# Optimization experiments

Hardware: AMD Instinct MI355X
Metric: run time of the kernel (lower is better)

## Reference

```python
import jax, jax.numpy as jnp
import numpy as np

B, L, D, H = 2, 2048, 1024, 16
HD = D // H
SCALE = HD ** (-0.5)


def setup_inputs() -> dict:
    key = jax.random.key(0)
    ks = jax.random.split(key, 12)
    mk = lambda k, shape: (0.02 * jax.random.normal(k, shape, dtype=jnp.float32))
    return {
        "x_real": jax.random.normal(ks[0], (B, L, D), dtype=jnp.float32),
        "x_imag": jax.random.normal(ks[1], (B, L, D), dtype=jnp.float32),
        "wq_r": mk(ks[2], (D, D)),
        "wq_i": mk(ks[3], (D, D)),
        "wk_r": mk(ks[4], (D, D)),
        "wk_i": mk(ks[5], (D, D)),
        "wv_r": mk(ks[6], (D, D)),
        "wv_i": mk(ks[7], (D, D)),
        "wo_r": mk(ks[8], (D, D)),
        "wo_i": mk(ks[9], (D, D)),
        "bo_r": jnp.zeros((D,), dtype=jnp.float32),
        "bo_i": jnp.zeros((D,), dtype=jnp.float32),
    }


def _clinear(xr, xi, wr, wi):
    # (a+bi)(c+di): real = a@Wr^T - b@Wi^T ; imag = a@Wi^T + b@Wr^T
    r = xr @ wr.T - xi @ wi.T
    i = xr @ wi.T + xi @ wr.T
    return r, i


def _heads(t):
    # [B,L,D] -> [B,H,L,hd]
    return t.reshape(B, L, H, HD).transpose(0, 2, 1, 3)


def reference(x_real, x_imag, wq_r, wq_i, wk_r, wk_i, wv_r, wv_i, wo_r, wo_i, bo_r, bo_i):
    Qr, Qi = _clinear(x_real, x_imag, wq_r, wq_i)
    Kr, Ki = _clinear(x_real, x_imag, wk_r, wk_i)
    Vr, Vi = _clinear(x_real, x_imag, wv_r, wv_i)
    Qr, Qi, Kr, Ki, Vr, Vi = map(_heads, (Qr, Qi, Kr, Ki, Vr, Vi))

    # real part of complex dot product: Re(Q)Re(K)^T + Im(Q)Im(K)^T
    scores = (jnp.einsum("bhqd,bhkd->bhqk", Qr, Kr)
              + jnp.einsum("bhqd,bhkd->bhqk", Qi, Ki)) * SCALE
    causal = jnp.tril(jnp.ones((L, L), dtype=bool))
    scores = jnp.where(causal, scores, -jnp.inf)
    w = jax.nn.softmax(scores, axis=-1)

    out_r = jnp.einsum("bhqk,bhkd->bhqd", w, Vr)
    out_i = jnp.einsum("bhqk,bhkd->bhqd", w, Vi)
    merge = lambda t: t.transpose(0, 2, 1, 3).reshape(B, L, D)
    out_r, out_i = merge(out_r), merge(out_i)

    yr, yi = _clinear(out_r, out_i, wo_r, wo_i)
    return yr + bo_r, yi + bo_i
```

## Files before the change

kernel.cpp:

```cpp
#include <hip/hip_runtime.h>
#include <hip/hip_bf16.h>


using f32x4  = __attribute__((ext_vector_type(4))) float;
using short8 = __attribute__((ext_vector_type(8))) short;
using bf16_t = __hip_bfloat16;

#define AS1 __attribute__((address_space(1)))
#define AS3 __attribute__((address_space(3)))

__device__ __forceinline__ void gload_lds16(const bf16_t* g, bf16_t* l) {
  __builtin_amdgcn_global_load_lds((const AS1 unsigned int*)g, (AS3 unsigned int*)l, 16, 0, 0);
}

__device__ __forceinline__ unsigned short bfbits(float f) {
  union { bf16_t h; unsigned short u; } c; c.h = __float2bfloat16(f); return c.u;
}

__global__ void pack_x_k(const float* __restrict__ xr, const float* __restrict__ xi,
                         bf16_t* __restrict__ out) {
  const int total4 = 4096 * 2048 / 4;
  for (int idx = blockIdx.x * blockDim.x + threadIdx.x; idx < total4;
       idx += gridDim.x * blockDim.x) {
    int m = idx >> 9, k = (idx & 511) * 4;
    const float* src = (k < 1024) ? (xr + (size_t)m * 1024 + k)
                                  : (xi + (size_t)m * 1024 + (k - 1024));
    float4 v = *(const float4*)src;
    unsigned int lo = (unsigned)bfbits(v.x) | ((unsigned)bfbits(v.y) << 16);
    unsigned int hi = (unsigned)bfbits(v.z) | ((unsigned)bfbits(v.w) << 16);
    *(uint2*)(out + (size_t)idx * 4) = make_uint2(lo, hi);
  }
}

__global__ void pack_wqkv_k(const float* __restrict__ wqr, const float* __restrict__ wqi,
                            const float* __restrict__ wkr, const float* __restrict__ wki,
                            const float* __restrict__ wvr, const float* __restrict__ wvi,
                            bf16_t* __restrict__ out) {
  const int total4 = 6144 * 2048 / 4;
  for (int idx = blockIdx.x * blockDim.x + threadIdx.x; idx < total4;
       idx += gridDim.x * blockDim.x) {
    int row = idx >> 9, k = (idx & 511) * 4;
    int sec = row >> 10, r1 = row & 1023;
    bool lowk = (k < 1024);
    int kk = lowk ? k : (k - 1024);
    const float* base = wqr; float sg = 1.f;
    switch (sec) {
      case 0: base = lowk ? wqr : wqi; sg = lowk ? 1.f : -1.f; break;
      case 1: base = lowk ? wqi : wqr; break;
      case 2: base = lowk ? wkr : wki; sg = lowk ? 1.f : -1.f; break;
      case 3: base = lowk ? wki : wkr; break;
      case 4: base = lowk ? wvr : wvi; sg = lowk ? 1.f : -1.f; break;
      case 5: base = lowk ? wvi : wvr; break;
    }
    float4 v = *(const float4*)(base + (size_t)r1 * 1024 + kk);
    unsigned int lo = (unsigned)bfbits(v.x * sg) | ((unsigned)bfbits(v.y * sg) << 16);
    unsigned int hi = (unsigned)bfbits(v.z * sg) | ((unsigned)bfbits(v.w * sg) << 16);
    *(uint2*)(out + (size_t)idx * 4) = make_uint2(lo, hi);
  }
}

__global__ void pack_wo_k(const float* __restrict__ wor, const float* __restrict__ woi,
                          bf16_t* __restrict__ out) {
  const int total4 = 2048 * 2048 / 4;
  for (int idx = blockIdx.x * blockDim.x + threadIdx.x; idx < total4;
       idx += gridDim.x * blockDim.x) {
    int row = idx >> 9, k = (idx & 511) * 4;
    int sec = row >> 10, r1 = row & 1023;
    bool lowk = (k < 1024);
    int kk = lowk ? k : (k - 1024);
    const float* base; float sg = 1.f;
    if (sec == 0) { base = lowk ? wor : woi; sg = lowk ? 1.f : -1.f; }
    else          { base = lowk ? woi : wor; }
    float4 v = *(const float4*)(base + (size_t)r1 * 1024 + kk);
    unsigned int lo = (unsigned)bfbits(v.x * sg) | ((unsigned)bfbits(v.y * sg) << 16);
    unsigned int hi = (unsigned)bfbits(v.z * sg) | ((unsigned)bfbits(v.w * sg) << 16);
    *(uint2*)(out + (size_t)idx * 4) = make_uint2(lo, hi);
  }
}

__device__ __forceinline__ void gemm_core(const bf16_t* __restrict__ A,
                                          const bf16_t* __restrict__ W,
                                          int m0, int n0, f32x4 (&acc)[4][4]) {
  __shared__ __align__(16) bf16_t sA[128 * 64];
  __shared__ __align__(16) bf16_t sB[128 * 64];
  const int tid = threadIdx.x;
  const int lane = tid & 63, w = tid >> 6;
  const int wr = w >> 1, wc = w & 1;
  const int quad = lane >> 4, m16 = lane & 15;
  const int srow = w * 32 + (lane >> 3);
  const int gcol = (((lane & 7) ^ (lane >> 3)) * 8);
  const int swz7 = m16 & 7;
  for (int k0 = 0; k0 < 2048; k0 += 64) {
    __syncthreads();
#pragma unroll
    for (int i = 0; i < 4; ++i) {
      gload_lds16(A + (size_t)(m0 + srow + i * 8) * 2048 + k0 + gcol,
                  sA + (size_t)(w * 32 + i * 8) * 64 + lane * 8);
      gload_lds16(W + (size_t)(n0 + srow + i * 8) * 2048 + k0 + gcol,
                  sB + (size_t)(w * 32 + i * 8) * 64 + lane * 8);
    }
    __syncthreads();
#pragma unroll
    for (int kk = 0; kk < 2; ++kk) {
      short8 af[4], bf[4];
#pragma unroll
      for (int i = 0; i < 4; ++i)
        af[i] = *(const short8*)(sA + (wr * 64 + i * 16 + m16) * 64 +
                                 ((kk * 4 + quad) ^ swz7) * 8);
#pragma unroll
      for (int j = 0; j < 4; ++j)
        bf[j] = *(const short8*)(sB + (wc * 64 + j * 16 + m16) * 64 +
                                 ((kk * 4 + quad) ^ swz7) * 8);
#pragma unroll
      for (int i = 0; i < 4; ++i)
#pragma unroll
        for (int j = 0; j < 4; ++j)
          acc[i][j] = __builtin_amdgcn_mfma_f32_16x16x32_bf16(af[i], bf[j], acc[i][j], 0, 0, 0);
    }
  }
}

__global__ __launch_bounds__(256) void gemm_qkv_k(const bf16_t* __restrict__ A,
                                                  const bf16_t* __restrict__ W,
                                                  bf16_t* __restrict__ qk,
                                                  bf16_t* __restrict__ vt) {
  f32x4 acc[4][4] = {};
  const int m0 = blockIdx.x * 128, n0 = blockIdx.y * 128;
  gemm_core(A, W, m0, n0, acc);
  const int lane = threadIdx.x & 63, w = threadIdx.x >> 6;
  const int wr = w >> 1, wc = w & 1, quad = lane >> 4, m16 = lane & 15;
#pragma unroll
  for (int i = 0; i < 4; ++i) {
    const int rowb = m0 + wr * 64 + i * 16 + quad * 4;
#pragma unroll
    for (int j = 0; j < 4; ++j) {
      const int col = n0 + wc * 64 + j * 16 + m16;
      if (col < 4096) {
        const float sc = (col < 2048) ? 0.125f : 1.f;
#pragma unroll
        for (int r = 0; r < 4; ++r)
          qk[(size_t)(rowb + r) * 4096 + col] = __float2bfloat16(acc[i][j][r] * sc);
      } else {
        const int vcol = col - 4096;
        const int ri = vcol >> 10, dfeat = vcol & 1023;
        const int b = rowb >> 11, seq = rowb & 2047;
        const size_t vrow = (size_t)(b * 2048 + (dfeat >> 6) * 128 + ri * 64 + (dfeat & 63));
        unsigned int lo = (unsigned)bfbits(acc[i][j][0]) | ((unsigned)bfbits(acc[i][j][1]) << 16);
        unsigned int hi = (unsigned)bfbits(acc[i][j][2]) | ((unsigned)bfbits(acc[i][j][3]) << 16);
        *(uint2*)(vt + vrow * 2048 + seq) = make_uint2(lo, hi);
      }
    }
  }
}

__global__ __launch_bounds__(256) void gemm_out_k(const bf16_t* __restrict__ A,
                                                  const bf16_t* __restrict__ W,
                                                  const float* __restrict__ bor,
                                                  const float* __restrict__ boi,
                                                  float* __restrict__ out) {
  f32x4 acc[4][4] = {};
  const int m0 = blockIdx.x * 128, n0 = blockIdx.y * 128;
  gemm_core(A, W, m0, n0, acc);
  const int lane = threadIdx.x & 63, w = threadIdx.x >> 6;
  const int wr = w >> 1, wc = w & 1, quad = lane >> 4, m16 = lane & 15;
#pragma unroll
  for (int i = 0; i < 4; ++i) {
    const int rowb = m0 + wr * 64 + i * 16 + quad * 4;
#pragma unroll
    for (int j = 0; j < 4; ++j) {
      const int col = n0 + wc * 64 + j * 16 + m16;
      float bias; float* op;
      if (col < 1024) { bias = bor[col]; op = out + col; }
      else            { bias = boi[col - 1024]; op = out + 4194304 + (col - 1024); }
#pragma unroll
      for (int r = 0; r < 4; ++r)
        op[(size_t)(rowb + r) * 1024] = acc[i][j][r] + bias;
    }
  }
}

__global__ __launch_bounds__(256, 2) void attn_k(const bf16_t* __restrict__ qk,
                                                 const bf16_t* __restrict__ vt,
                                                 bf16_t* __restrict__ acat) {
  __shared__ __align__(16) bf16_t sK[64 * 128];
  __shared__ __align__(16) bf16_t sV[144 * 64];
  __shared__ __align__(16) bf16_t sP[4][2][16 * 72];
  const int tid = threadIdx.x, lane = tid & 63, w = tid >> 6;
  const int quad = lane >> 4, m16 = lane & 15;
  const int x = blockIdx.x, bh = blockIdx.y, b = bh >> 4, h = bh & 15;
  const size_t qkrow0 = (size_t)b * 2048;
  const int qA = x * 64, qB = (31 - x) * 64;
  const int nT = 32 - x;
  const int swz7 = m16 & 7;

  {
    const int rr = tid >> 4, cb = (tid & 15) * 4;
    const bf16_t v = __float2bfloat16(rr == 0 ? 1.f : 0.f);
#pragma unroll
    for (int i = 0; i < 4; ++i) sV[(128 + rr) * 64 + cb + i] = v;
  }

  short8 qfA[4], qfB[4];
  {
    const bf16_t* qa = qk + (qkrow0 + qA + w * 16 + m16) * 4096;
    const bf16_t* qb = qk + (qkrow0 + qB + w * 16 + m16) * 4096;
#pragma unroll
    for (int kk = 0; kk < 4; ++kk) {
      const int col = (kk >> 1) * 1024 + h * 64 + (kk & 1) * 32 + quad * 8;
      qfA[kk] = *(const short8*)(qa + col);
      qfB[kk] = *(const short8*)(qb + col);
    }
  }
  f32x4 oA[9], oB[9];
#pragma unroll
  for (int j = 0; j < 9; ++j) { oA[j] = (f32x4){0.f,0.f,0.f,0.f}; oB[j] = (f32x4){0.f,0.f,0.f,0.f}; }

  const int qrowA = qA + w * 16 + quad * 4;
  const int qrowB = qB + w * 16 + quad * 4;

  const int kl4 = lane >> 4, kl15 = lane & 15;
  const int vl3 = lane >> 3;
  const int vg7 = ((lane & 7) ^ vl3) * 8;

  for (int t = 0; t < nT; ++t) {
    const int k0 = t * 64;
    __syncthreads();
#pragma unroll
    for (int i = 0; i < 4; ++i) {
      const int row = w * 16 + i * 4 + kl4;
      const int g = kl15 ^ (row & 7);
      const int col = 2048 + (g >> 3) * 1024 + h * 64 + (g & 7) * 8;
      gload_lds16(qk + (qkrow0 + k0 + row) * 4096 + col,
                  sK + (size_t)(w * 16 + i * 4) * 128 + lane * 8);
    }
#pragma unroll
    for (int i = 0; i < 4; ++i) {
      const int row = w * 32 + i * 8 + vl3;
      gload_lds16(vt + ((size_t)bh * 128 + row) * 2048 + k0 + vg7,
                  sV + (size_t)(w * 32 + i * 8) * 64 + lane * 8);
    }
    __syncthreads();

    const bool aAct = (t <= x);
    const bool dgA = (t == x), dgB = (t == nT - 1);

    f32x4 sAv[4], sBv[4];
    if (aAct) {
#pragma unroll
      for (int jt = 0; jt < 4; ++jt) {
        f32x4 a1 = (f32x4){0.f,0.f,0.f,0.f}, a2 = (f32x4){0.f,0.f,0.f,0.f};
#pragma unroll
        for (int kk = 0; kk < 4; ++kk) {
          short8 kf = *(const short8*)(sK + (jt * 16 + m16) * 128 +
                                       ((kk * 4 + quad) ^ swz7) * 8);
          a1 = __builtin_amdgcn_mfma_f32_16x16x32_bf16(qfA[kk], kf, a1, 0, 0, 0);
          a2 = __builtin_amdgcn_mfma_f32_16x16x32_bf16(qfB[kk], kf, a2, 0, 0, 0);
        }
        sAv[jt] = a1; sBv[jt] = a2;
      }
    } else {
#pragma unroll
      for (int jt = 0; jt < 4; ++jt) {
        f32x4 a2 = (f32x4){0.f,0.f,0.f,0.f};
#pragma unroll
        for (int kk = 0; kk < 4; ++kk) {
          short8 kf = *(const short8*)(sK + (jt * 16 + m16) * 128 +
                                       ((kk * 4 + quad) ^ swz7) * 8);
          a2 = __builtin_amdgcn_mfma_f32_16x16x32_bf16(qfB[kk], kf, a2, 0, 0, 0);
        }
        sBv[jt] = a2;
      }
    }

    if (aAct) {
      bf16_t* pw = sP[w][0];
#pragma unroll
      for (int jt = 0; jt < 4; ++jt)
#pragma unroll
        for (int r = 0; r < 4; ++r) {
          float s = sAv[jt][r];
          if (dgA && (k0 + jt * 16 + m16 > qrowA + r)) s = -1e30f;
          pw[(quad * 4 + r) * 72 + jt * 16 + m16] = __float2bfloat16(__expf(s));
        }
    }
    {
      bf16_t* pw = sP[w][1];
#pragma unroll
      for (int jt = 0; jt < 4; ++jt)
#pragma unroll
        for (int r = 0; r < 4; ++r) {
          float s = sBv[jt][r];
          if (dgB && (k0 + jt * 16 + m16 > qrowB + r)) s = -1e30f;
          pw[(quad * 4 + r) * 72 + jt * 16 + m16] = __float2bfloat16(__expf(s));
        }
    }
    asm volatile("s_waitcnt lgkmcnt(0)" ::: "memory");

    if (aAct) {
#pragma unroll
      for (int kc = 0; kc < 2; ++kc) {
        short8 pA = *(const short8*)(sP[w][0] + m16 * 72 + kc * 32 + quad * 8);
        short8 pB = *(const short8*)(sP[w][1] + m16 * 72 + kc * 32 + quad * 8);
#pragma unroll
        for (int j = 0; j < 9; ++j) {
          short8 vf = *(const short8*)(sV + (j * 16 + m16) * 64 +
                                       ((kc * 4 + quad) ^ swz7) * 8);
          oA[j] = __builtin_amdgcn_mfma_f32_16x16x32_bf16(pA, vf, oA[j], 0, 0, 0);
          oB[j] = __builtin_amdgcn_mfma_f32_16x16x32_bf16(pB, vf, oB[j], 0, 0, 0);
        }
      }
    } else {
#pragma unroll
      for (int kc = 0; kc < 2; ++kc) {
        short8 pB = *(const short8*)(sP[w][1] + m16 * 72 + kc * 32 + quad * 8);
#pragma unroll
        for (int j = 0; j < 9; ++j) {
          short8 vf = *(const short8*)(sV + (j * 16 + m16) * 64 +
                                       ((kc * 4 + quad) ^ swz7) * 8);
          oB[j] = __builtin_amdgcn_mfma_f32_16x16x32_bf16(pB, vf, oB[j], 0, 0, 0);
        }
      }
    }
  }

#pragma unroll
  for (int part = 0; part < 2; ++part) {
    f32x4* o = part ? oB : oA;
    const int qrow = part ? qrowB : qrowA;
    float inv[4];
#pragma unroll
    for (int r = 0; r < 4; ++r)
      inv[r] = 1.f / __shfl(o[8][r], lane & 48);
#pragma unroll
    for (int j = 0; j < 8; ++j) {
      const int d = j * 16 + m16;
      const int col = (d < 64) ? (h * 64 + d) : (1024 + h * 64 + (d - 64));
#pragma unroll
      for (int r = 0; r < 4; ++r)
        acat[((size_t)b * 2048 + qrow + r) * 2048 + col] = __float2bfloat16(o[j][r] * inv[r]);
    }
  }
}

extern "C" void kernel_launch(void* const* d_in, const int* in_sizes, int n_in,
                              void* d_out, int out_size, void* d_ws, size_t ws_size,
                              hipStream_t stream) {
  const float* xr  = (const float*)d_in[0];
  const float* xi  = (const float*)d_in[1];
  const float* wqr = (const float*)d_in[2];
  const float* wqi = (const float*)d_in[3];
  const float* wkr = (const float*)d_in[4];
  const float* wki = (const float*)d_in[5];
  const float* wvr = (const float*)d_in[6];
  const float* wvi = (const float*)d_in[7];
  const float* wor = (const float*)d_in[8];
  const float* woi = (const float*)d_in[9];
  const float* bor = (const float*)d_in[10];
  const float* boi = (const float*)d_in[11];
  float* out = (float*)d_out;

  char* ws = (char*)d_ws;
  bf16_t* Xcat = (bf16_t*)(ws);
  bf16_t* Wqkv = (bf16_t*)(ws + 16777216ull);
  bf16_t* QKb  = (bf16_t*)(ws + 41943040ull);
  bf16_t* Vt   = (bf16_t*)(ws + 75497472ull);
  bf16_t* Acat = (bf16_t*)(ws + 92274688ull);
  bf16_t* Wo   = (bf16_t*)(ws + 109051904ull);

  pack_x_k<<<2048, 256, 0, stream>>>(xr, xi, Xcat);
  pack_wqkv_k<<<2048, 256, 0, stream>>>(wqr, wqi, wkr, wki, wvr, wvi, Wqkv);
  pack_wo_k<<<1024, 256, 0, stream>>>(wor, woi, Wo);
  gemm_qkv_k<<<dim3(32, 48), 256, 0, stream>>>(Xcat, Wqkv, QKb, Vt);
  attn_k<<<dim3(16, 32), 256, 0, stream>>>(QKb, Vt, Acat);
  gemm_out_k<<<dim3(32, 16), 256, 0, stream>>>(Acat, Wo, bor, boi, out);
}
```

Baseline: 396.3 us.

## Split paired causal query tiles across separate waves in 512-thread attention blocks

Result: faster. 362.0 us (-8.6%).

```diff
diff --git a/kernel.cpp b/kernel.cpp
--- a/kernel.cpp
+++ b/kernel.cpp
@@ -179,44 +179,43 @@
   }
 }
 
-__global__ __launch_bounds__(256, 2) void attn_k(const bf16_t* __restrict__ qk,
+__global__ __launch_bounds__(512, 4) void attn_k(const bf16_t* __restrict__ qk,
                                                  const bf16_t* __restrict__ vt,
                                                  bf16_t* __restrict__ acat) {
   __shared__ __align__(16) bf16_t sK[64 * 128];
   __shared__ __align__(16) bf16_t sV[144 * 64];
-  __shared__ __align__(16) bf16_t sP[4][2][16 * 72];
+  __shared__ __align__(16) bf16_t sP[8][16 * 72];
   const int tid = threadIdx.x, lane = tid & 63, w = tid >> 6;
+  const int wq = w & 3, sub = w >> 2;
   const int quad = lane >> 4, m16 = lane & 15;
   const int x = blockIdx.x, bh = blockIdx.y, b = bh >> 4, h = bh & 15;
   const size_t qkrow0 = (size_t)b * 2048;
   const int qA = x * 64, qB = (31 - x) * 64;
   const int nT = 32 - x;
   const int swz7 = m16 & 7;
-
-  {
+  const int qbase = (sub ? qB : qA) + wq * 16;
+
+  if (tid < 256) {
     const int rr = tid >> 4, cb = (tid & 15) * 4;
     const bf16_t v = __float2bfloat16(rr == 0 ? 1.f : 0.f);
 #pragma unroll
     for (int i = 0; i < 4; ++i) sV[(128 + rr) * 64 + cb + i] = v;
   }
 
-  short8 qfA[4], qfB[4];
+  short8 qf[4];
   {
-    const bf16_t* qa = qk + (qkrow0 + qA + w * 16 + m16) * 4096;
-    const bf16_t* qb = qk + (qkrow0 + qB + w * 16 + m16) * 4096;
+    const bf16_t* qa = qk + (qkrow0 + qbase + m16) * 4096;
 #pragma unroll
     for (int kk = 0; kk < 4; ++kk) {
       const int col = (kk >> 1) * 1024 + h * 64 + (kk & 1) * 32 + quad * 8;
-      qfA[kk] = *(const short8*)(qa + col);
-      qfB[kk] = *(const short8*)(qb + col);
-    }
-  }
-  f32x4 oA[9], oB[9];
-#pragma unroll
-  for (int j = 0; j < 9; ++j) { oA[j] = (f32x4){0.f,0.f,0.f,0.f}; oB[j] = (f32x4){0.f,0.f,0.f,0.f}; }
-
-  const int qrowA = qA + w * 16 + quad * 4;
-  const int qrowB = qB + w * 16 + quad * 4;
+      qf[kk] = *(const short8*)(qa + col);
+    }
+  }
+  f32x4 o[9];
+#pragma unroll
+  for (int j = 0; j < 9; ++j) o[j] = (f32x4){0.f, 0.f, 0.f, 0.f};
+
+  const int qrow = qbase + quad * 4;
 
   const int kl4 = lane >> 4, kl15 = lane & 15;
   const int vl3 = lane >> 3;
@@ -226,119 +225,73 @@
     const int k0 = t * 64;
     __syncthreads();
 #pragma unroll
-    for (int i = 0; i < 4; ++i) {
-      const int row = w * 16 + i * 4 + kl4;
+    for (int i = 0; i < 2; ++i) {
+      const int row = w * 8 + i * 4 + kl4;
       const int g = kl15 ^ (row & 7);
       const int col = 2048 + (g >> 3) * 1024 + h * 64 + (g & 7) * 8;
       gload_lds16(qk + (qkrow0 + k0 + row) * 4096 + col,
-                  sK + (size_t)(w * 16 + i * 4) * 128 + lane * 8);
-    }
-#pragma unroll
-    for (int i = 0; i < 4; ++i) {
-      const int row = w * 32 + i * 8 + vl3;
+                  sK + (size_t)(w * 8 + i * 4) * 128 + lane * 8);
+    }
+#pragma unroll
+    for (int i = 0; i < 2; ++i) {
+      const int row = w * 16 + i * 8 + vl3;
       gload_lds16(vt + ((size_t)bh * 128 + row) * 2048 + k0 + vg7,
-                  sV + (size_t)(w * 32 + i * 8) * 64 + lane * 8);
+                  sV + (size_t)(w * 16 + i * 8) * 64 + lane * 8);
     }
     __syncthreads();
 
-    const bool aAct = (t <= x);
-    const bool dgA = (t == x), dgB = (t == nT - 1);
-
-    f32x4 sAv[4], sBv[4];
-    if (aAct) {
+    const bool act = sub ? true : (t <= x);
+    if (act) {
+      const bool dg = sub ? (t == nT - 1) : (t == x);
+
+      f32x4 sv[4];
 #pragma unroll
       for (int jt = 0; jt < 4; ++jt) {
-        f32x4 a1 = (f32x4){0.f,0.f,0.f,0.f}, a2 = (f32x4){0.f,0.f,0.f,0.f};
+        f32x4 a = (f32x4){0.f, 0.f, 0.f, 0.f};
 #pragma unroll
         for (int kk = 0; kk < 4; ++kk) {
           short8 kf = *(const short8*)(sK + (jt * 16 + m16) * 128 +
                                        ((kk * 4 + quad) ^ swz7) * 8);
-          a1 = __builtin_amdgcn_mfma_f32_16x16x32_bf16(qfA[kk], kf, a1, 0, 0, 0);
-          a2 = __builtin_amdgcn_mfma_f32_16x16x32_bf16(qfB[kk], kf, a2, 0, 0, 0);
+          a = __builtin_amdgcn_mfma_f32_16x16x32_bf16(qf[kk], kf, a, 0, 0, 0);
         }
-        sAv[jt] = a1; sBv[jt] = a2;
+        sv[jt] = a;
       }
-    } else {
-#pragma unroll
-      for (int jt = 0; jt < 4; ++jt) {
-        f32x4 a2 = (f32x4){0.f,0.f,0.f,0.f};
-#pragma unroll
-        for (int kk = 0; kk < 4; ++kk) {
-          short8 kf = *(const short8*)(sK + (jt * 16 + m16) * 128 +
-                                       ((kk * 4 + quad) ^ swz7) * 8);
-          a2 = __builtin_amdgcn_mfma_f32_16x16x32_bf16(qfB[kk], kf, a2, 0, 0, 0);
-        }
-        sBv[jt] = a2;
-      }
-    }
-
-    if (aAct) {
-      bf16_t* pw = sP[w][0];
+
+      bf16_t* pw = sP[w];
 #pragma unroll
       for (int jt = 0; jt < 4; ++jt)
 #pragma unroll
         for (int r = 0; r < 4; ++r) {
-          float s = sAv[jt][r];
-          if (dgA && (k0 + jt * 16 + m16 > qrowA + r)) s = -1e30f;
+          float s = sv[jt][r];
+          if (dg && (k0 + jt * 16 + m16 > qrow + r)) s = -1e30f;
           pw[(quad * 4 + r) * 72 + jt * 16 + m16] = __float2bfloat16(__expf(s));
         }
-    }
-    {
-      bf16_t* pw = sP[w][1];
-#pragma unroll
-      for (int jt = 0; jt < 4; ++jt)
-#pragma unroll
-        for (int r = 0; r < 4; ++r) {
-          float s = sBv[jt][r];
-          if (dgB && (k0 + jt * 16 + m16 > qrowB + r)) s = -1e30f;
-          pw[(quad * 4 + r) * 72 + jt * 16 + m16] = __float2bfloat16(__expf(s));
-        }
-    }
-    asm volatile("s_waitcnt lgkmcnt(0)" ::: "memory");
-
-    if (aAct) {
+      asm volatile("s_waitcnt lgkmcnt(0)" ::: "memory");
+
 #pragma unroll
       for (int kc = 0; kc < 2; ++kc) {
-        short8 pA = *(const short8*)(sP[w][0] + m16 * 72 + kc * 32 + quad * 8);
-        short8 pB = *(const short8*)(sP[w][1] + m16 * 72 + kc * 32 + quad * 8);
+        short8 p = *(const short8*)(pw + m16 * 72 + kc * 32 + quad * 8);
 #pragma unroll
         for (int j = 0; j < 9; ++j) {
           short8 vf = *(const short8*)(sV + (j * 16 + m16) * 64 +
                                        ((kc * 4 + quad) ^ swz7) * 8);
-          oA[j] = __builtin_amdgcn_mfma_f32_16x16x32_bf16(pA, vf, oA[j], 0, 0, 0);
-          oB[j] = __builtin_amdgcn_mfma_f32_16x16x32_bf16(pB, vf, oB[j], 0, 0, 0);
+          o[j] = __builtin_amdgcn_mfma_f32_16x16x32_bf16(p, vf, o[j], 0, 0, 0);
         }
       }
-    } else {
-#pragma unroll
-      for (int kc = 0; kc < 2; ++kc) {
-        short8 pB = *(const short8*)(sP[w][1] + m16 * 72 + kc * 32 + quad * 8);
-#pragma unroll
-        for (int j = 0; j < 9; ++j) {
-          short8 vf = *(const short8*)(sV + (j * 16 + m16) * 64 +
-                                       ((kc * 4 + quad) ^ swz7) * 8);
-          oB[j] = __builtin_amdgcn_mfma_f32_16x16x32_bf16(pB, vf, oB[j], 0, 0, 0);
-        }
-      }
-    }
-  }
-
-#pragma unroll
-  for (int part = 0; part < 2; ++part) {
-    f32x4* o = part ? oB : oA;
-    const int qrow = part ? qrowB : qrowA;
-    float inv[4];
+    }
+  }
+
+  float inv[4];
+#pragma unroll
+  for (int r = 0; r < 4; ++r)
+    inv[r] = 1.f / __shfl(o[8][r], lane & 48);
+#pragma unroll
+  for (int j = 0; j < 8; ++j) {
+    const int d = j * 16 + m16;
+    const int col = (d < 64) ? (h * 64 + d) : (1024 + h * 64 + (d - 64));
 #pragma unroll
     for (int r = 0; r < 4; ++r)
-      inv[r] = 1.f / __shfl(o[8][r], lane & 48);
-#pragma unroll
-    for (int j = 0; j < 8; ++j) {
-      const int d = j * 16 + m16;
-      const int col = (d < 64) ? (h * 64 + d) : (1024 + h * 64 + (d - 64));
-#pragma unroll
-      for (int r = 0; r < 4; ++r)
-        acat[((size_t)b * 2048 + qrow + r) * 2048 + col] = __float2bfloat16(o[j][r] * inv[r]);
-    }
+      acat[((size_t)b * 2048 + qrow + r) * 2048 + col] = __float2bfloat16(o[j][r] * inv[r]);
   }
 }
 
@@ -371,6 +324,6 @@
   pack_wqkv_k<<<2048, 256, 0, stream>>>(wqr, wqi, wkr, wki, wvr, wvi, Wqkv);
   pack_wo_k<<<1024, 256, 0, stream>>>(wor, woi, Wo);
   gemm_qkv_k<<<dim3(32, 48), 256, 0, stream>>>(Xcat, Wqkv, QKb, Vt);
-  attn_k<<<dim3(16, 32), 256, 0, stream>>>(QKb, Vt, Acat);
+  attn_k<<<dim3(16, 32), 512, 0, stream>>>(QKb, Vt, Acat);
   gemm_out_k<<<dim3(32, 16), 256, 0, stream>>>(Acat, Wo, bor, boi, out);
 }
```
